# Optimization experiments

Measured on AMD Instinct MI355X. Metric: run time of the kernel, lower is better.

Reference implementation:

```python
import jax, jax.numpy as jnp
import numpy as np

R = 128            # coarse grid resolution (hash-grid domain)
SCALE = 2          # scale_factor
VS_COARSE = 1.0    # coarse voxel size
VS_FINE = VS_COARSE / SCALE
N_IN = 400_000
C = 32

# 8 trilinear corner offsets, fixed
CORNERS = np.stack(np.meshgrid([0, 1], [0, 1], [0, 1], indexing='ij'), -1).reshape(-1, 3)


def setup_inputs() -> dict:
    key = jax.random.key(0)
    k1, k2 = jax.random.split(key)
    coarse_coords = jax.random.randint(k1, (N_IN, 3), 0, R, dtype=jnp.int32)
    feat = jax.random.normal(k2, (N_IN, C), dtype=jnp.float32)
    # fine grid = subdivided coarse grid: each coarse voxel -> SCALE^3 children
    offs = jnp.stack(
        jnp.meshgrid(jnp.arange(SCALE), jnp.arange(SCALE), jnp.arange(SCALE), indexing='ij'),
        -1).reshape(-1, 3).astype(jnp.int32)  # [8,3]
    fine_coords = (coarse_coords[:, None, :] * SCALE + offs[None]).reshape(-1, 3)  # [8*N_IN,3]
    return {"feat": feat, "coarse_coords": coarse_coords, "fine_coords": fine_coords}


def reference(feat, coarse_coords, fine_coords):
    """Trilinear upsample: sample coarse sparse-voxel features at fine voxel centers.
    Emulates in_grid.sample_trilinear(out_grid.grid_to_world(active_coords), feat).
    Hash-grid lookup is emulated with a dense index volume; missing neighbors
    contribute zero feature (standard sparse-grid convention).
    """
    n_in = feat.shape[0]
    # build coord -> row index volume (stand-in for the voxel hash map)
    table = -jnp.ones((R, R, R), jnp.int32)
    table = table.at[coarse_coords[:, 0], coarse_coords[:, 1], coarse_coords[:, 2]].set(
        jnp.arange(n_in, dtype=jnp.int32))
    # fine voxel centers in world space (centers at (ijk+0.5)*voxel_size)
    out_pos = (fine_coords.astype(jnp.float32) + 0.5) * VS_FINE          # [M,3]
    # continuous coarse-grid coords; coarse centers at (i+0.5)*VS_COARSE
    g = out_pos / VS_COARSE - 0.5                                        # [M,3]
    base = jnp.floor(g)
    frac = g - base                                                      # [M,3]
    corners = jnp.asarray(CORNERS, jnp.int32)                            # [8,3]
    cc = base.astype(jnp.int32)[:, None, :] + corners[None]              # [M,8,3]
    inb = jnp.all((cc >= 0) & (cc < R), axis=-1)                         # [M,8]
    ccc = jnp.clip(cc, 0, R - 1)
    idx = table[ccc[..., 0], ccc[..., 1], ccc[..., 2]]                   # [M,8]
    valid = inb & (idx >= 0)
    # trilinear weights: prod over xyz of frac or (1-frac)
    w3 = jnp.where(corners[None].astype(jnp.float32) > 0,
                   frac[:, None, :], 1.0 - frac[:, None, :])             # [M,8,3]
    w = jnp.prod(w3, axis=-1) * valid.astype(jnp.float32)                # [M,8]
    f = feat[jnp.clip(idx, 0, n_in - 1)]                                 # [M,8,C]
    return jnp.einsum('mk,mkc->mc', w, f)                                # [M,C]
```

## Files before the change

kernel.cpp:

```cpp
#include <hip/hip_runtime.h>


#define R 128
#define TABLE_ELEMS (R * R * R)

typedef float f32x4 __attribute__((ext_vector_type(4)));

__global__ void build_table_kernel(const int* __restrict__ coarse,
                                   int* __restrict__ table, int n) {
    int i = blockIdx.x * blockDim.x + threadIdx.x;
    if (i >= n) return;
    int x = coarse[i * 3 + 0];
    int y = coarse[i * 3 + 1];
    int z = coarse[i * 3 + 2];
    atomicMax(&table[(x * R + y) * R + z], i);
}

__device__ __forceinline__ void gload_lds16(const f32x4* g, f32x4* l) {
    __builtin_amdgcn_global_load_lds(
        (const __attribute__((address_space(1))) void*)g,
        (__attribute__((address_space(3))) void*)l, 16, 0, 0);
}

__global__ void __launch_bounds__(256)
upsample_kernel(const f32x4* __restrict__ feat4,
                const int* __restrict__ coarse,
                const int* __restrict__ table,
                f32x4* __restrict__ out4,
                int n_in) {
    __shared__ f32x4 sm[4][2][256];

    int wib  = threadIdx.x >> 6;
    int lane = threadIdx.x & 63;
    int half = lane >> 5;
    int pl   = lane & 31;

    int viA = __builtin_amdgcn_readfirstlane(blockIdx.x * 8 + wib * 2);
    if (viA >= n_in) return;
    int viB = viA + 1;

    int vi_p = half ? viB : viA;
    int myidx = -1;
    if (pl < 27 && vi_p < n_in) {
        int cx = coarse[vi_p * 3 + 0];
        int cy = coarse[vi_p * 3 + 1];
        int cz = coarse[vi_p * 3 + 2];
        int dx  = pl / 9;
        int rem = pl - dx * 9;
        int dy  = rem / 3;
        int dz  = rem - dy * 3;
        int x = cx + dx - 1, y = cy + dy - 1, z = cz + dz - 1;
        if ((unsigned)x < (unsigned)R && (unsigned)y < (unsigned)R &&
            (unsigned)z < (unsigned)R)
            myidx = table[(x * R + y) * R + z];
    }
    unsigned long long vmask = __ballot(myidx >= 0);
    unsigned maskA = (unsigned)(vmask & 0x7FFFFFFull);
    unsigned maskB = (unsigned)((vmask >> 32) & 0x7FFFFFFull);

    int g    = lane >> 3;
    int part = lane & 7;
    f32x4* smA = &sm[wib][0][0];
    f32x4* smB = &sm[wib][1][0];
#pragma unroll
    for (int r = 0; r < 4; ++r) {
        int idx = __shfl(myidx, r * 8 + g);
        if (idx >= 0)
            gload_lds16(&feat4[(size_t)idx * 8 + part], smA + r * 64);
    }
#pragma unroll
    for (int r = 0; r < 4; ++r) {
        int idx = __shfl(myidx, 32 + r * 8 + g);
        if (idx >= 0)
            gload_lds16(&feat4[(size_t)idx * 8 + part], smB + r * 64);
    }
    asm volatile("s_waitcnt vmcnt(0)" ::: "memory");
    __builtin_amdgcn_sched_barrier(0);

    int ox = (g >> 2) & 1, oy = (g >> 1) & 1, oz = g & 1;
    float wx0 = 0.25f + 0.5f * (float)ox, wx1 = 0.75f - 0.5f * (float)ox;
    float wy0 = 0.25f + 0.5f * (float)oy, wy1 = 0.75f - 0.5f * (float)oy;
    float wz0 = 0.25f + 0.5f * (float)oz, wz1 = 0.75f - 0.5f * (float)oz;

    f32x4 accA = (f32x4)(0.f);
    f32x4 accB = (f32x4)(0.f);
#pragma unroll
    for (int k = 0; k < 8; ++k) {
        int kx = (k >> 2) & 1, ky = (k >> 1) & 1, kz = k & 1;
        int nb = (ox + kx) * 9 + (oy + ky) * 3 + (oz + kz);
        float w = (kx ? wx1 : wx0) * (ky ? wy1 : wy0) * (kz ? wz1 : wz0);
        if ((maskA >> nb) & 1u) accA += w * smA[nb * 8 + part];
        if ((maskB >> nb) & 1u) accB += w * smB[nb * 8 + part];
    }

    __builtin_nontemporal_store(accA, &out4[(size_t)viA * 64 + lane]);
    if (viB < n_in)
        __builtin_nontemporal_store(accB, &out4[(size_t)viB * 64 + lane]);
}

extern "C" void kernel_launch(void* const* d_in, const int* in_sizes, int n_in_arrs,
                              void* d_out, int out_size, void* d_ws, size_t ws_size,
                              hipStream_t stream) {
    const float* feat = (const float*)d_in[0];
    const int* coarse = (const int*)d_in[1];

    int n_in = in_sizes[1] / 3;
    int* table = (int*)d_ws;

    hipMemsetAsync(table, 0xFF, (size_t)TABLE_ELEMS * sizeof(int), stream);

    build_table_kernel<<<(n_in + 255) / 256, 256, 0, stream>>>(coarse, table, n_in);

    int nblocks = (n_in + 7) / 8;
    upsample_kernel<<<nblocks, 256, 0, stream>>>(
        (const f32x4*)feat, coarse, table, (f32x4*)d_out, n_in);
}
```

Measured before the change: 567.5 us.

## Compact valid neighbor features into fewer LDS slots to raise occupancy

Neighbor features are now loaded into registers and then written to LDS in compacted order, ranked by a popcount over the validity mask. This replaces the direct global-to-LDS loads that reserved all 27 neighbor slots. LDS per block halves, and launch bounds ask for 8 blocks per CU to allow more resident waves. The cost is losing the async direct-to-LDS path, added register pressure from staging eight vectors, and extra popcount and select logic. Neighbors ranked beyond 16 fall back to a direct global read.

```diff
diff --git a/kernel.cpp b/kernel.cpp
--- a/kernel.cpp
+++ b/kernel.cpp
@@ -3,6 +3,7 @@
 
 #define R 128
 #define TABLE_ELEMS (R * R * R)
+#define NSLOT 16
 
 typedef float f32x4 __attribute__((ext_vector_type(4)));
 
@@ -16,19 +17,13 @@
     atomicMax(&table[(x * R + y) * R + z], i);
 }
 
-__device__ __forceinline__ void gload_lds16(const f32x4* g, f32x4* l) {
-    __builtin_amdgcn_global_load_lds(
-        (const __attribute__((address_space(1))) void*)g,
-        (__attribute__((address_space(3))) void*)l, 16, 0, 0);
-}
-
-__global__ void __launch_bounds__(256)
+__global__ void __launch_bounds__(256, 8)
 upsample_kernel(const f32x4* __restrict__ feat4,
                 const int* __restrict__ coarse,
                 const int* __restrict__ table,
                 f32x4* __restrict__ out4,
                 int n_in) {
-    __shared__ f32x4 sm[4][2][256];
+    __shared__ f32x4 sm[4][2][NSLOT * 8];
 
     int wib  = threadIdx.x >> 6;
     int lane = threadIdx.x & 63;
@@ -60,21 +55,49 @@
 
     int g    = lane >> 3;
     int part = lane & 7;
+
+    f32x4 fA0, fA1, fA2, fA3, fB0, fB1, fB2, fB3;
+    {
+        int i0 = __shfl(myidx, 0 * 8 + g);
+        int i1 = __shfl(myidx, 1 * 8 + g);
+        int i2 = __shfl(myidx, 2 * 8 + g);
+        int i3 = __shfl(myidx, 3 * 8 + g);
+        if (i0 >= 0) fA0 = feat4[(size_t)i0 * 8 + part];
+        if (i1 >= 0) fA1 = feat4[(size_t)i1 * 8 + part];
+        if (i2 >= 0) fA2 = feat4[(size_t)i2 * 8 + part];
+        if (i3 >= 0) fA3 = feat4[(size_t)i3 * 8 + part];
+        int j0 = __shfl(myidx, 32 + 0 * 8 + g);
+        int j1 = __shfl(myidx, 32 + 1 * 8 + g);
+        int j2 = __shfl(myidx, 32 + 2 * 8 + g);
+        int j3 = __shfl(myidx, 32 + 3 * 8 + g);
+        if (j0 >= 0) fB0 = feat4[(size_t)j0 * 8 + part];
+        if (j1 >= 0) fB1 = feat4[(size_t)j1 * 8 + part];
+        if (j2 >= 0) fB2 = feat4[(size_t)j2 * 8 + part];
+        if (j3 >= 0) fB3 = feat4[(size_t)j3 * 8 + part];
+    }
+
     f32x4* smA = &sm[wib][0][0];
     f32x4* smB = &sm[wib][1][0];
 #pragma unroll
     for (int r = 0; r < 4; ++r) {
-        int idx = __shfl(myidx, r * 8 + g);
-        if (idx >= 0)
-            gload_lds16(&feat4[(size_t)idx * 8 + part], smA + r * 64);
+        int s = r * 8 + g;
+        unsigned bit = (s < 27) ? (1u << s) : 0u;
+        if (maskA & bit) {
+            int rk = __popc(maskA & (bit - 1u));
+            if (rk < NSLOT) {
+                f32x4 v = (r == 0) ? fA0 : (r == 1) ? fA1 : (r == 2) ? fA2 : fA3;
+                smA[rk * 8 + part] = v;
+            }
+        }
+        if (maskB & bit) {
+            int rk = __popc(maskB & (bit - 1u));
+            if (rk < NSLOT) {
+                f32x4 v = (r == 0) ? fB0 : (r == 1) ? fB1 : (r == 2) ? fB2 : fB3;
+                smB[rk * 8 + part] = v;
+            }
+        }
     }
-#pragma unroll
-    for (int r = 0; r < 4; ++r) {
-        int idx = __shfl(myidx, 32 + r * 8 + g);
-        if (idx >= 0)
-            gload_lds16(&feat4[(size_t)idx * 8 + part], smB + r * 64);
-    }
-    asm volatile("s_waitcnt vmcnt(0)" ::: "memory");
+    asm volatile("s_waitcnt lgkmcnt(0)" ::: "memory");
     __builtin_amdgcn_sched_barrier(0);
 
     int ox = (g >> 2) & 1, oy = (g >> 1) & 1, oz = g & 1;
@@ -88,9 +111,28 @@
     for (int k = 0; k < 8; ++k) {
         int kx = (k >> 2) & 1, ky = (k >> 1) & 1, kz = k & 1;
         int nb = (ox + kx) * 9 + (oy + ky) * 3 + (oz + kz);
+        unsigned bit = 1u << nb;
         float w = (kx ? wx1 : wx0) * (ky ? wy1 : wy0) * (kz ? wz1 : wz0);
-        if ((maskA >> nb) & 1u) accA += w * smA[nb * 8 + part];
-        if ((maskB >> nb) & 1u) accB += w * smB[nb * 8 + part];
+        if (maskA & bit) {
+            int rk = __popc(maskA & (bit - 1u));
+            f32x4 f;
+            if (rk < NSLOT) f = smA[rk * 8 + part];
+            else {
+                int idx = __shfl(myidx, nb);
+                f = feat4[(size_t)idx * 8 + part];
+            }
+            accA += w * f;
+        }
+        if (maskB & bit) {
+            int rk = __popc(maskB & (bit - 1u));
+            f32x4 f;
+            if (rk < NSLOT) f = smB[rk * 8 + part];
+            else {
+                int idx = __shfl(myidx, 32 + nb);
+                f = feat4[(size_t)idx * 8 + part];
+            }
+            accB += w * f;
+        }
     }
 
     __builtin_nontemporal_store(accA, &out4[(size_t)viA * 64 + lane]);
```

After: 569.1 us. No clear change (+0.3%).
